# Optimization experiments

Measured on AMD Instinct MI355X. Metric: run time of the kernel, lower is better.

The kernel has to match this reference:

```python
import jax, jax.numpy as jnp
import numpy as np

LMAX = 10
F_IN = 64
F_OUT = 64
N_GRID = 512
IRREP_DIM = sum((2 * l + 1) ** 2 for l in range(LMAX + 1))  # 1771
BATCH = 256


def setup_inputs() -> dict:
    key = jax.random.key(0)
    kx, kD, kw = jax.random.split(key, 3)
    x = jax.random.normal(kx, (BATCH, F_IN, IRREP_DIM), dtype=jnp.float32)
    D = jax.random.normal(kD, (N_GRID, IRREP_DIM), dtype=jnp.float32)
    w = jax.random.normal(kw, (F_IN, F_OUT, N_GRID), dtype=jnp.float32)
    return {"x": x, "D": D, "w": w}


def _so3_linear(x, psi):
    # x:   (B, f_in, sum_l (2l+1)^2) signal over SO(3) irreps
    # psi: (f_in, f_out, sum_l (2l+1)^2) per-degree block weights
    B, f_in, _ = x.shape
    f_out = psi.shape[1]
    outs = []
    off = 0
    for l in range(LMAX + 1):
        d = 2 * l + 1
        blk = d * d
        # input block: multiplicity u (=d) x irrep component m (=d)
        x_l = x[:, :, off:off + blk].reshape(B, f_in, d, d)        # (B,i,u,m)
        w_l = psi[:, :, off:off + blk].reshape(f_in, f_out, d, d)  # (i,o,u,v)
        alpha = 1.0 / np.sqrt(f_in * d)  # e3nn fan-in path normalization
        out_l = jnp.einsum('bium,iouv->bovm', x_l, w_l) * alpha
        outs.append(out_l.reshape(B, f_out, blk))
        off += blk
    return jnp.concatenate(outs, axis=-1)


def reference(x, D, w):
    # project spatial filter into Fourier (irrep) domain
    n_grid = D.shape[0]
    psi = jnp.einsum('ni,xyn->xyi', D, w) / np.sqrt(n_grid)  # (f_in, f_out, IRREP_DIM)
    return _so3_linear(x, psi)
```

## Files before the change

kernel.cpp:

```cpp
#include <hip/hip_runtime.h>
#include <hip/hip_bf16.h>

#define IDIM 1771
#define NF 64
#define NG 512

constexpr int OFFS[12] = {0, 1, 10, 35, 84, 165, 286, 455, 680, 969, 1330, 1771};

typedef float f32x4 __attribute__((ext_vector_type(4)));
typedef float f32x2 __attribute__((ext_vector_type(2)));
typedef __bf16 bf16x2 __attribute__((ext_vector_type(2)));
typedef __bf16 bf16x8 __attribute__((ext_vector_type(8)));

__device__ __forceinline__ void gl_lds16(const void* g, void* l) {
    __builtin_amdgcn_global_load_lds((const __attribute__((address_space(1))) void*)g,
                                     (__attribute__((address_space(3))) void*)l, 16, 0, 0);
}

__global__ __launch_bounds__(256) void prep_repack_kernel(const float* __restrict__ D,
                                                          const float* __restrict__ w,
                                                          const float* __restrict__ x,
                                                          __bf16* __restrict__ Dt,
                                                          __bf16* __restrict__ wb,
                                                          __hip_bfloat16* __restrict__ A) {
    __shared__ alignas(16) char smem[16640];
    const int blk = blockIdx.x;
    const int t = threadIdx.x;
    const int lane = t & 63, grp = t >> 6;

    if (blk < 224) {
        float (*T)[65] = (float (*)[65])smem;
        const int ct = blk >> 3, nt = blk & 7;
        const int c0 = ct * 64, n0 = nt * 64;
        for (int nn = grp; nn < 64; nn += 4) {
            int c = c0 + lane;
            T[nn][lane] = (c < IDIM) ? D[(n0 + nn) * IDIM + c] : 0.0f;
        }
        __syncthreads();
        for (int cc = grp; cc < 64; cc += 4) {
            int c = c0 + cc;
            if (c < IDIM) Dt[c * NG + n0 + lane] = (__bf16)T[lane][cc];
        }
    } else if (blk < 288) {
        const int o = blk - 224;
#pragma unroll 4
        for (int ii = 0; ii < 64; ++ii) {
            f32x2 v = *(const f32x2*)&w[((size_t)(ii * 64 + o)) * NG + t * 2];
            bf16x2 ov;
            ov.x = (__bf16)v.x;
            ov.y = (__bf16)v.y;
            *(bf16x2*)&wb[((size_t)(o * 64 + ii)) * NG + t * 2] = ov;
        }
    } else {
        const int idx = blk - 288;
        const int l = idx >> 8;
        const int b = idx & 255;
        const int d = 2 * l + 1, off = OFFS[l], csq = d * d, Kp = 64 * d;
        __bf16 (*T)[66] = (__bf16 (*)[66])smem;
        const float* xb = x + (size_t)b * NF * IDIM + off;
        __bf16* Ab = (__bf16*)(A + (size_t)16384 * off + (size_t)b * d * Kp);

        for (int c0 = 0; c0 < csq; c0 += 64) {
            for (int ii = grp; ii < 64; ii += 4) {
                int c = c0 + lane;
                float v = (c < csq) ? xb[ii * IDIM + c] : 0.0f;
                T[ii][lane] = (__bf16)v;
            }
            __syncthreads();
#pragma unroll
            for (int s = 0; s < 2; ++s) {
                int idx2 = s * 256 + t;
                int c_loc = idx2 >> 3, i0 = (idx2 & 7) * 8;
                int c = c0 + c_loc;
                if (c < csq) {
                    int u = (unsigned)c / (unsigned)d;
                    int m = c - u * d;
                    bf16x8 v;
#pragma unroll
                    for (int j = 0; j < 8; ++j) v[j] = T[i0 + j][c_loc];
                    *(bf16x8*)(Ab + (size_t)m * Kp + u * 64 + i0) = v;
                }
            }
            __syncthreads();
        }
    }
}

__global__ __launch_bounds__(256) void psi_mfma_kernel(const __bf16* __restrict__ Dt,
                                                       const __bf16* __restrict__ wb,
                                                       __bf16* __restrict__ Bm) {
    __shared__ alignas(16) __bf16 S[4][4096];

    const int t = threadIdx.x, w = t >> 6, ln = t & 63;
    const int row0 = blockIdx.x * 128;
    const int col0 = blockIdx.y * 128;

    const __bf16* gp[4];
    __bf16* lp[4];
#pragma unroll
    for (int q = 0; q < 4; ++q) {
        int chunk = w * 4 + q;
        bool isA = chunk < 8;
        int j = chunk & 7;
        int r16 = j * 16 + (ln >> 2);
        int g = isA ? (row0 + r16 < IDIM ? row0 + r16 : IDIM - 1) : (col0 + r16);
        gp[q] = (isA ? Dt : wb) + (size_t)g * NG + (ln & 3) * 8;
        lp[q] = S[isA ? 0 : 1] + j * 512;
    }

    f32x4 acc[4][4];
    f32x4 zero = {0.0f, 0.0f, 0.0f, 0.0f};
#pragma unroll
    for (int i = 0; i < 4; ++i)
#pragma unroll
        for (int j = 0; j < 4; ++j) acc[i][j] = zero;

    const int wr = (w >> 1) * 64, wc = (w & 1) * 64;
    const int fr = ln & 15, kh = ln >> 4;

#pragma unroll
    for (int q = 0; q < 4; ++q) { gl_lds16(gp[q], lp[q]); gp[q] += 32; }
    asm volatile("s_waitcnt vmcnt(0)" ::: "memory");
    __builtin_amdgcn_s_barrier();
    __builtin_amdgcn_sched_barrier(0);

    int cur = 0;
    for (int kt = 0; kt < NG; kt += 32) {
        if (kt + 32 < NG) {
#pragma unroll
            for (int q = 0; q < 4; ++q) {
                gl_lds16(gp[q], lp[q] + (cur ^ 1) * 8192);
                gp[q] += 32;
            }
        }
        const __bf16* As_ = S[cur * 2];
        const __bf16* Bs_ = S[cur * 2 + 1];
        bf16x8 af[4], bfr[4];
#pragma unroll
        for (int mt = 0; mt < 4; ++mt)
            af[mt] = *(const bf16x8*)&As_[(wr + mt * 16 + fr) * 32 + kh * 8];
#pragma unroll
        for (int nt = 0; nt < 4; ++nt)
            bfr[nt] = *(const bf16x8*)&Bs_[(wc + nt * 16 + fr) * 32 + kh * 8];
#pragma unroll
        for (int mt = 0; mt < 4; ++mt)
#pragma unroll
            for (int nt = 0; nt < 4; ++nt)
                acc[mt][nt] = __builtin_amdgcn_mfma_f32_16x16x32_bf16(af[mt], bfr[nt],
                                                                      acc[mt][nt], 0, 0, 0);
        asm volatile("s_waitcnt vmcnt(0)" ::: "memory");
        __builtin_amdgcn_s_barrier();
        __builtin_amdgcn_sched_barrier(0);
        cur ^= 1;
    }

    const float s = 0.04419417382415922f;
    const int o = (col0 + wc) >> 6;
#pragma unroll
    for (int mt = 0; mt < 4; ++mt) {
#pragma unroll
        for (int e = 0; e < 4; ++e) {
            int c = row0 + wr + mt * 16 + kh * 4 + e;
            if (c < IDIM) {
                int l = 0;
#pragma unroll
                for (int ll = 1; ll < 11; ++ll)
                    if (c >= OFFS[ll]) l = ll;
                int d = 2 * l + 1, off = OFFS[l];
                int rem = c - off;
                int u = (unsigned)rem / (unsigned)d;
                int v = rem - u * d;
                __bf16* bb = Bm + (size_t)4096 * off + (size_t)(o * d + v) * (64 * d) + u * 64;
#pragma unroll
                for (int nt = 0; nt < 4; ++nt) {
                    int i = nt * 16 + fr;
                    bb[i] = (__bf16)(acc[mt][nt][e] * s);
                }
            }
        }
    }
}

__global__ __launch_bounds__(256) void so3_gemm_all(const __bf16* __restrict__ A,
                                                    const __bf16* __restrict__ Bm,
                                                    float* __restrict__ out) {
    const int bid = blockIdx.x;
    const int v_ = (bid & 7) * 237 + (bid >> 3);
    if (v_ >= 1892) return;

    int l = 10, base = 0;
    if (v_ >= 462)  { l = 9; base = 462; }
    if (v_ >= 842)  { l = 8; base = 842; }
    if (v_ >= 1148) { l = 7; base = 1148; }
    if (v_ >= 1388) { l = 6; base = 1388; }
    if (v_ >= 1570) { l = 5; base = 1570; }
    if (v_ >= 1702) { l = 4; base = 1702; }
    if (v_ >= 1792) { l = 3; base = 1792; }
    if (v_ >= 1848) { l = 2; base = 1848; }
    if (v_ >= 1878) { l = 1; base = 1878; }
    if (v_ >= 1890) { l = 0; base = 1890; }

    const int d = 2 * l + 1;
    const int off = OFFS[l];
    const int Np = 64 * d, Kp = 64 * d;
    const int ntiles = l + 1;
    const int rel = v_ - base;
    const int bx = (unsigned)rel / (unsigned)ntiles;
    const int by = rel - bx * ntiles;
    const int row0 = bx * 128, col0 = by * 128;

    constexpr float ALPHA[11] = {0.125f, 0.07216878f, 0.05590170f, 0.04724556f,
                                 0.04166667f, 0.03768892f, 0.03466879f, 0.03227486f,
                                 0.03031695f, 0.02867697f, 0.02727724f};

    __shared__ alignas(16) __bf16 S[4][4096];

    const int t = threadIdx.x, w = t >> 6, ln = t & 63;

    const __bf16* Abase = A + (size_t)16384 * off;
    const __bf16* Bbase = Bm + (size_t)4096 * off;

    const __bf16* gp[4];
    __bf16* lp[4];
#pragma unroll
    for (int q = 0; q < 4; ++q) {
        int chunk = w * 4 + q;
        bool isA = chunk < 8;
        int j = chunk & 7;
        int r16 = j * 16 + (ln >> 2);
        int g = isA ? (row0 + r16) : (col0 + r16 < Np ? col0 + r16 : Np - 1);
        gp[q] = (isA ? Abase : Bbase) + (size_t)g * Kp + (ln & 3) * 8;
        lp[q] = S[isA ? 0 : 1] + j * 512;
    }

    f32x4 acc[4][4];
    f32x4 zero = {0.0f, 0.0f, 0.0f, 0.0f};
#pragma unroll
    for (int i = 0; i < 4; ++i)
#pragma unroll
        for (int j = 0; j < 4; ++j) acc[i][j] = zero;

    const int wr = (w >> 1) * 64, wc = (w & 1) * 64;
    const int fr = ln & 15, kh = ln >> 4;

#pragma unroll
    for (int q = 0; q < 4; ++q) { gl_lds16(gp[q], lp[q]); gp[q] += 32; }
    asm volatile("s_waitcnt vmcnt(0)" ::: "memory");
    __builtin_amdgcn_s_barrier();
    __builtin_amdgcn_sched_barrier(0);

    int cur = 0;
    for (int kt = 0; kt < Kp; kt += 32) {
        if (kt + 32 < Kp) {
#pragma unroll
            for (int q = 0; q < 4; ++q) {
                gl_lds16(gp[q], lp[q] + (cur ^ 1) * 8192);
                gp[q] += 32;
            }
        }
        const __bf16* As_ = S[cur * 2];
        const __bf16* Bs_ = S[cur * 2 + 1];
        bf16x8 af[4], bfr[4];
#pragma unroll
        for (int mt = 0; mt < 4; ++mt)
            af[mt] = *(const bf16x8*)&As_[(wr + mt * 16 + fr) * 32 + kh * 8];
#pragma unroll
        for (int nt = 0; nt < 4; ++nt)
            bfr[nt] = *(const bf16x8*)&Bs_[(wc + nt * 16 + fr) * 32 + kh * 8];
#pragma unroll
        for (int mt = 0; mt < 4; ++mt)
#pragma unroll
            for (int nt = 0; nt < 4; ++nt)
                acc[mt][nt] = __builtin_amdgcn_mfma_f32_16x16x32_bf16(af[mt], bfr[nt],
                                                                      acc[mt][nt], 0, 0, 0);
        asm volatile("s_waitcnt vmcnt(0)" ::: "memory");
        __builtin_amdgcn_s_barrier();
        __builtin_amdgcn_sched_barrier(0);
        cur ^= 1;
    }

    __syncthreads();
    float* Tw = (float*)S + w * 256;
    const float alpha = ALPHA[l];

#pragma unroll
    for (int mt = 0; mt < 4; ++mt) {
        int r = row0 + wr + mt * 16 + fr;
        int b = (unsigned)r / (unsigned)d;
        int m = r - b * d;
        float* ob = out + (size_t)b * NF * IDIM + off + m;
#pragma unroll
        for (int nt = 0; nt < 4; ++nt) {
#pragma unroll
            for (int e = 0; e < 4; ++e) Tw[(kh * 4 + e) * 16 + fr] = acc[mt][nt][e];
            f32x4 vals = *(const f32x4*)&Tw[fr * 16 + kh * 4];
            int qb = col0 + wc + nt * 16 + kh * 4;
            int o = (unsigned)qb / (unsigned)d;
            int vv = qb - o * d;
#pragma unroll
            for (int j = 0; j < 4; ++j) {
                if (qb + j < Np) ob[o * IDIM + vv * d] = alpha * vals[j];
                ++vv;
                if (vv == d) { vv = 0; ++o; }
            }
        }
    }
}

extern "C" void kernel_launch(void* const* d_in, const int* in_sizes, int n_in,
                              void* d_out, int out_size, void* d_ws, size_t ws_size,
                              hipStream_t stream) {
    const float* x = (const float*)d_in[0];
    const float* D = (const float*)d_in[1];
    const float* w = (const float*)d_in[2];
    float* out = (float*)d_out;

    char* ws = (char*)d_ws;
    const size_t DT_BYTES = (size_t)IDIM * NG * 2;
    const size_t WB_BYTES = (size_t)4096 * NG * 2;
    const size_t A_BYTES = (size_t)16384 * IDIM * 2;

    __bf16* Dt = (__bf16*)ws;
    __bf16* wb = (__bf16*)(ws + DT_BYTES);
    __hip_bfloat16* A = (__hip_bfloat16*)(ws + DT_BYTES + WB_BYTES);
    __bf16* Bm = (__bf16*)(ws + DT_BYTES + WB_BYTES + A_BYTES);

    prep_repack_kernel<<<3104, 256, 0, stream>>>(D, w, x, Dt, wb, A);
    psi_mfma_kernel<<<dim3(14, 32), 256, 0, stream>>>(Dt, wb, Bm);
    so3_gemm_all<<<1896, 256, 0, stream>>>((const __bf16*)A, Bm, out);
}
```

Before: 395.4 us.

## Triple-buffer LDS pipeline in GEMM kernels and batch loads in repack

Both MFMA GEMM kernels move from a double-buffered LDS scheme that waited on all loads each step to a three-stage ring. Two tiles stay in flight, and the wait is a partial vmcnt(4) followed by one barrier per step. The aim is to hide global-load latency behind MFMA work. The prep/repack kernel now issues its global loads into registers in batches before writing to LDS, which raises memory-level parallelism. The cost is 48KB of LDS per block instead of 32KB, which can lower occupancy.

```diff
diff --git a/kernel.cpp b/kernel.cpp
--- a/kernel.cpp
+++ b/kernel.cpp
@@ -32,10 +32,15 @@
         float (*T)[65] = (float (*)[65])smem;
         const int ct = blk >> 3, nt = blk & 7;
         const int c0 = ct * 64, n0 = nt * 64;
-        for (int nn = grp; nn < 64; nn += 4) {
+        float tmp[16];
+#pragma unroll
+        for (int p = 0; p < 16; ++p) {
+            int nn = grp + p * 4;
             int c = c0 + lane;
-            T[nn][lane] = (c < IDIM) ? D[(n0 + nn) * IDIM + c] : 0.0f;
-        }
+            tmp[p] = (c < IDIM) ? D[(size_t)(n0 + nn) * IDIM + c] : 0.0f;
+        }
+#pragma unroll
+        for (int p = 0; p < 16; ++p) T[grp + p * 4][lane] = tmp[p];
         __syncthreads();
         for (int cc = grp; cc < 64; cc += 4) {
             int c = c0 + cc;
@@ -43,13 +48,19 @@
         }
     } else if (blk < 288) {
         const int o = blk - 224;
-#pragma unroll 4
-        for (int ii = 0; ii < 64; ++ii) {
-            f32x2 v = *(const f32x2*)&w[((size_t)(ii * 64 + o)) * NG + t * 2];
-            bf16x2 ov;
-            ov.x = (__bf16)v.x;
-            ov.y = (__bf16)v.y;
-            *(bf16x2*)&wb[((size_t)(o * 64 + ii)) * NG + t * 2] = ov;
+#pragma unroll
+        for (int ii0 = 0; ii0 < 64; ii0 += 8) {
+            f32x2 tmp[8];
+#pragma unroll
+            for (int j = 0; j < 8; ++j)
+                tmp[j] = *(const f32x2*)&w[((size_t)((ii0 + j) * 64 + o)) * NG + t * 2];
+#pragma unroll
+            for (int j = 0; j < 8; ++j) {
+                bf16x2 ov;
+                ov.x = (__bf16)tmp[j].x;
+                ov.y = (__bf16)tmp[j].y;
+                *(bf16x2*)&wb[((size_t)(o * 64 + ii0 + j)) * NG + t * 2] = ov;
+            }
         }
     } else {
         const int idx = blk - 288;
@@ -61,11 +72,15 @@
         __bf16* Ab = (__bf16*)(A + (size_t)16384 * off + (size_t)b * d * Kp);
 
         for (int c0 = 0; c0 < csq; c0 += 64) {
-            for (int ii = grp; ii < 64; ii += 4) {
+            float tmp[16];
+#pragma unroll
+            for (int p = 0; p < 16; ++p) {
+                int ii = grp + p * 4;
                 int c = c0 + lane;
-                float v = (c < csq) ? xb[ii * IDIM + c] : 0.0f;
-                T[ii][lane] = (__bf16)v;
-            }
+                tmp[p] = (c < csq) ? xb[(size_t)ii * IDIM + c] : 0.0f;
+            }
+#pragma unroll
+            for (int p = 0; p < 16; ++p) T[grp + p * 4][lane] = (__bf16)tmp[p];
             __syncthreads();
 #pragma unroll
             for (int s = 0; s < 2; ++s) {
@@ -89,7 +104,7 @@
 __global__ __launch_bounds__(256) void psi_mfma_kernel(const __bf16* __restrict__ Dt,
                                                        const __bf16* __restrict__ wb,
                                                        __bf16* __restrict__ Bm) {
-    __shared__ alignas(16) __bf16 S[4][4096];
+    __shared__ alignas(16) __bf16 S[3 * 8192];
 
     const int t = threadIdx.x, w = t >> 6, ln = t & 63;
     const int row0 = blockIdx.x * 128;
@@ -105,7 +120,7 @@
         int r16 = j * 16 + (ln >> 2);
         int g = isA ? (row0 + r16 < IDIM ? row0 + r16 : IDIM - 1) : (col0 + r16);
         gp[q] = (isA ? Dt : wb) + (size_t)g * NG + (ln & 3) * 8;
-        lp[q] = S[isA ? 0 : 1] + j * 512;
+        lp[q] = S + (isA ? 0 : 4096) + j * 512;
     }
 
     f32x4 acc[4][4];
@@ -118,23 +133,32 @@
     const int wr = (w >> 1) * 64, wc = (w & 1) * 64;
     const int fr = ln & 15, kh = ln >> 4;
 
-#pragma unroll
-    for (int q = 0; q < 4; ++q) { gl_lds16(gp[q], lp[q]); gp[q] += 32; }
-    asm volatile("s_waitcnt vmcnt(0)" ::: "memory");
-    __builtin_amdgcn_s_barrier();
-    __builtin_amdgcn_sched_barrier(0);
-
-    int cur = 0;
-    for (int kt = 0; kt < NG; kt += 32) {
-        if (kt + 32 < NG) {
-#pragma unroll
-            for (int q = 0; q < 4; ++q) {
-                gl_lds16(gp[q], lp[q] + (cur ^ 1) * 8192);
-                gp[q] += 32;
-            }
-        }
-        const __bf16* As_ = S[cur * 2];
-        const __bf16* Bs_ = S[cur * 2 + 1];
+    auto STAGE = [&](int bi) {
+#pragma unroll
+        for (int q = 0; q < 4; ++q) {
+            gl_lds16(gp[q], lp[q] + bi * 8192);
+            gp[q] += 32;
+        }
+    };
+
+    const int nsteps = NG / 32;
+    STAGE(0);
+    STAGE(1);
+
+    int bi = 0;
+    for (int s = 0; s < nsteps; ++s) {
+        if (s + 1 < nsteps) asm volatile("s_waitcnt vmcnt(4)" ::: "memory");
+        else                asm volatile("s_waitcnt vmcnt(0)" ::: "memory");
+        __builtin_amdgcn_s_barrier();
+        __builtin_amdgcn_sched_barrier(0);
+        if (s + 2 < nsteps) {
+            int nb = s + 2 - ((s + 2) >= 3 ? 3 : 0);
+            nb = (s + 2) % 3;
+            STAGE(nb);
+        }
+        __builtin_amdgcn_sched_barrier(0);
+        const __bf16* As_ = S + bi * 8192;
+        const __bf16* Bs_ = S + bi * 8192 + 4096;
         bf16x8 af[4], bfr[4];
 #pragma unroll
         for (int mt = 0; mt < 4; ++mt)
@@ -148,13 +172,10 @@
             for (int nt = 0; nt < 4; ++nt)
                 acc[mt][nt] = __builtin_amdgcn_mfma_f32_16x16x32_bf16(af[mt], bfr[nt],
                                                                       acc[mt][nt], 0, 0, 0);
-        asm volatile("s_waitcnt vmcnt(0)" ::: "memory");
-        __builtin_amdgcn_s_barrier();
-        __builtin_amdgcn_sched_barrier(0);
-        cur ^= 1;
-    }
-
-    const float s = 0.04419417382415922f;
+        bi = (bi == 2) ? 0 : bi + 1;
+    }
+
+    const float sc = 0.04419417382415922f;
     const int o = (col0 + wc) >> 6;
 #pragma unroll
     for (int mt = 0; mt < 4; ++mt) {
@@ -174,7 +195,7 @@
 #pragma unroll
                 for (int nt = 0; nt < 4; ++nt) {
                     int i = nt * 16 + fr;
-                    bb[i] = (__bf16)(acc[mt][nt][e] * s);
+                    bb[i] = (__bf16)(acc[mt][nt][e] * sc);
                 }
             }
         }
@@ -213,7 +234,7 @@
                                  0.04166667f, 0.03768892f, 0.03466879f, 0.03227486f,
                                  0.03031695f, 0.02867697f, 0.02727724f};
 
-    __shared__ alignas(16) __bf16 S[4][4096];
+    __shared__ alignas(16) __bf16 S[3 * 8192];
 
     const int t = threadIdx.x, w = t >> 6, ln = t & 63;
 
@@ -230,7 +251,7 @@
         int r16 = j * 16 + (ln >> 2);
         int g = isA ? (row0 + r16) : (col0 + r16 < Np ? col0 + r16 : Np - 1);
         gp[q] = (isA ? Abase : Bbase) + (size_t)g * Kp + (ln & 3) * 8;
-        lp[q] = S[isA ? 0 : 1] + j * 512;
+        lp[q] = S + (isA ? 0 : 4096) + j * 512;
     }
 
     f32x4 acc[4][4];
@@ -243,23 +264,28 @@
     const int wr = (w >> 1) * 64, wc = (w & 1) * 64;
     const int fr = ln & 15, kh = ln >> 4;
 
-#pragma unroll
-    for (int q = 0; q < 4; ++q) { gl_lds16(gp[q], lp[q]); gp[q] += 32; }
-    asm volatile("s_waitcnt vmcnt(0)" ::: "memory");
-    __builtin_amdgcn_s_barrier();
-    __builtin_amdgcn_sched_barrier(0);
-
-    int cur = 0;
-    for (int kt = 0; kt < Kp; kt += 32) {
-        if (kt + 32 < Kp) {
-#pragma unroll
-            for (int q = 0; q < 4; ++q) {
-                gl_lds16(gp[q], lp[q] + (cur ^ 1) * 8192);
-                gp[q] += 32;
-            }
-        }
-        const __bf16* As_ = S[cur * 2];
-        const __bf16* Bs_ = S[cur * 2 + 1];
+    auto STAGE = [&](int bi) {
+#pragma unroll
+        for (int q = 0; q < 4; ++q) {
+            gl_lds16(gp[q], lp[q] + bi * 8192);
+            gp[q] += 32;
+        }
+    };
+
+    const int nsteps = Kp / 32;
+    STAGE(0);
+    STAGE(1);
+
+    int bi = 0;
+    for (int s = 0; s < nsteps; ++s) {
+        if (s + 1 < nsteps) asm volatile("s_waitcnt vmcnt(4)" ::: "memory");
+        else                asm volatile("s_waitcnt vmcnt(0)" ::: "memory");
+        __builtin_amdgcn_s_barrier();
+        __builtin_amdgcn_sched_barrier(0);
+        if (s + 2 < nsteps) STAGE((s + 2) % 3);
+        __builtin_amdgcn_sched_barrier(0);
+        const __bf16* As_ = S + bi * 8192;
+        const __bf16* Bs_ = S + bi * 8192 + 4096;
         bf16x8 af[4], bfr[4];
 #pragma unroll
         for (int mt = 0; mt < 4; ++mt)
@@ -273,10 +299,7 @@
             for (int nt = 0; nt < 4; ++nt)
                 acc[mt][nt] = __builtin_amdgcn_mfma_f32_16x16x32_bf16(af[mt], bfr[nt],
                                                                       acc[mt][nt], 0, 0, 0);
-        asm volatile("s_waitcnt vmcnt(0)" ::: "memory");
-        __builtin_amdgcn_s_barrier();
-        __builtin_amdgcn_sched_barrier(0);
-        cur ^= 1;
+        bi = (bi == 2) ? 0 : bi + 1;
     }
 
     __syncthreads();
```

Result: no change. 392.4 us (-0.7%).
